# Optimization experiments

Measured on AMD Instinct MI355X. Metric: run time of the kernel, lower is better.

The kernel has to match this reference:

```python
import jax, jax.numpy as jnp
import numpy as np

TOP_K = 2
NUM_EXPERTS = 8


def setup_inputs() -> dict:
    key = jax.random.key(0)
    ks = jax.random.split(key, 8)
    B, S, H, F, E = 2, 2048, 1024, 4096, NUM_EXPERTS
    x = jax.random.normal(ks[0], (B, S, H), dtype=jnp.float32)
    # Router linear (TopKRouter): hidden -> num_experts
    Wr = jax.random.normal(ks[1], (H, E), dtype=jnp.float32) * 0.02
    br = jnp.zeros((E,), dtype=jnp.float32)
    # Per-expert FeedForwardExpert: Linear(H,F) -> relu -> Linear(F,H), stacked over experts
    W1 = jax.random.normal(ks[2], (E, H, F), dtype=jnp.float32) * 0.02
    b1 = jnp.zeros((E, F), dtype=jnp.float32)
    W2 = jax.random.normal(ks[3], (E, F, H), dtype=jnp.float32) * 0.02
    b2 = jnp.zeros((E, H), dtype=jnp.float32)
    return {"x": x, "Wr": Wr, "br": br, "W1": W1, "b1": b1, "W2": W2, "b2": b2}


def reference(x, Wr, br, W1, b1, W2, b2):
    """MoELayer.forward (eval mode, no dropout, capacity assumed sufficient so
    no random token dropping -- dropping in the original is randperm-based).
    Top-2 routing with renormalized top-k softmax probs, weighted combine."""
    B, S, H = x.shape
    E = Wr.shape[1]
    xf = x.reshape(-1, H)                                   # [T, H]
    logits = xf @ Wr + br                                   # [T, E]
    probs = jax.nn.softmax(logits, axis=-1)
    top_vals, top_idx = jax.lax.top_k(probs, TOP_K)         # [T, k]
    weights = top_vals / jnp.sum(top_vals, axis=-1, keepdims=True)
    # combine weight per (token, expert): sum over k slots assigned to e
    onehot = jax.nn.one_hot(top_idx, E, dtype=xf.dtype)     # [T, k, E]
    combine = jnp.einsum('tk,tke->te', weights, onehot)     # [T, E]
    out = jnp.zeros_like(xf)
    for e in range(E):  # small fixed loop over experts
        h = jax.nn.relu(xf @ W1[e] + b1[e]) @ W2[e] + b2[e]  # [T, H]
        out = out + combine[:, e:e + 1] * h
    return out.reshape(B, S, H)
```

## Files before the change

kernel.cpp:

```cpp
#include <hip/hip_runtime.h>

#define T_TOK 4096
#define H_DIM 1024
#define F_DIM 4096
#define E_NUM 8
#define R_TOT 8192
#define NT_MAX 72
#define R_CAP (NT_MAX * 128)

typedef short bf16x8 __attribute__((ext_vector_type(8)));
typedef float f32x4 __attribute__((ext_vector_type(4)));

__device__ inline unsigned int f2bf_u(float f) {
  unsigned int u = __builtin_bit_cast(unsigned int, f);
  return (u + 0x7FFFu + ((u >> 16) & 1u)) >> 16;
}
__device__ inline unsigned short f2bf(float f) { return (unsigned short)f2bf_u(f); }

__device__ inline void async16(const void* g, void* l) {
  __builtin_amdgcn_global_load_lds((const __attribute__((address_space(1))) void*)g,
                                   (__attribute__((address_space(3))) void*)l, 16, 0, 0);
}

__global__ __launch_bounds__(256) void prep_router_k(
    const float* __restrict__ W1, const float* __restrict__ W2,
    unsigned short* __restrict__ WT1, unsigned short* __restrict__ WT2,
    const float* __restrict__ x, const float* __restrict__ Wr,
    const float* __restrict__ br, int* __restrict__ ctrl,
    int* __restrict__ t2i, float* __restrict__ t2w) {
  int bid = blockIdx.x;
  if (bid < 1024) {
    int lane = threadIdx.x & 63;
    int wid  = threadIdx.x >> 6;
    int t = bid * 4 + wid;
    const float* xr = x + (size_t)t * H_DIM;
    double acc[E_NUM];
#pragma unroll
    for (int e = 0; e < E_NUM; e++) acc[e] = 0.0;
    for (int i = lane; i < H_DIM; i += 64) {
      float xv = xr[i];
      const float* wr = Wr + (size_t)i * E_NUM;
      float4 w0 = *(const float4*)wr;
      float4 w1 = *(const float4*)(wr + 4);
      acc[0] += (double)xv * w0.x; acc[1] += (double)xv * w0.y;
      acc[2] += (double)xv * w0.z; acc[3] += (double)xv * w0.w;
      acc[4] += (double)xv * w1.x; acc[5] += (double)xv * w1.y;
      acc[6] += (double)xv * w1.z; acc[7] += (double)xv * w1.w;
    }
#pragma unroll
    for (int e = 0; e < E_NUM; e++) {
      double v = acc[e];
      for (int off = 32; off > 0; off >>= 1) v += __shfl_down(v, off);
      acc[e] = v;
    }
    if (lane == 0) {
      float l[E_NUM];
#pragma unroll
      for (int e = 0; e < E_NUM; e++) l[e] = (float)acc[e] + br[e];
      int ia = 0; float la = l[0];
#pragma unroll
      for (int e = 1; e < E_NUM; e++) if (l[e] > la) { la = l[e]; ia = e; }
      int ib = -1; float lb = -3.4e38f;
#pragma unroll
      for (int e = 0; e < E_NUM; e++) if (e != ia && l[e] > lb) { lb = l[e]; ib = e; }
      float w0 = 1.f / (1.f + __expf(lb - la));
      float w1 = 1.f - w0;
      t2i[2 * t] = ia; t2i[2 * t + 1] = ib;
      t2w[2 * t] = w0; t2w[2 * t + 1] = w1;
      atomicAdd(&ctrl[ia], 1);
      atomicAdd(&ctrl[ib], 1);
    }
    return;
  }
  int b2 = bid - 1024;
  size_t mat = (size_t)H_DIM * F_DIM;
  const float* in; unsigned short* out; int R, C, c0, r0;
  if (b2 < 8192) {
    int e = b2 >> 10, t = b2 & 1023;
    in = W1 + e * mat; out = WT1 + e * mat; R = H_DIM; C = F_DIM;
    c0 = (t & 63) * 64; r0 = (t >> 6) * 64;
  } else {
    int b3 = b2 - 8192;
    int e = b3 >> 10, t = b3 & 1023;
    in = W2 + e * mat; out = WT2 + e * mat; R = F_DIM; C = H_DIM;
    c0 = (t & 15) * 64; r0 = (t >> 4) * 64;
  }
  __shared__ unsigned int tile32[32][66];
  {
    int rp = threadIdx.x >> 3;
    int tc = (threadIdx.x & 7) * 8;
    const float* s0 = in + (size_t)(r0 + 2 * rp) * C + c0 + tc;
    const float* s1 = s0 + C;
    float4 a0 = *(const float4*)s0, a1 = *(const float4*)(s0 + 4);
    float4 b0 = *(const float4*)s1, b1 = *(const float4*)(s1 + 4);
    uint4 u0, u1;
    u0.x = f2bf_u(a0.x) | (f2bf_u(b0.x) << 16);
    u0.y = f2bf_u(a0.y) | (f2bf_u(b0.y) << 16);
    u0.z = f2bf_u(a0.z) | (f2bf_u(b0.z) << 16);
    u0.w = f2bf_u(a0.w) | (f2bf_u(b0.w) << 16);
    u1.x = f2bf_u(a1.x) | (f2bf_u(b1.x) << 16);
    u1.y = f2bf_u(a1.y) | (f2bf_u(b1.y) << 16);
    u1.z = f2bf_u(a1.z) | (f2bf_u(b1.z) << 16);
    u1.w = f2bf_u(a1.w) | (f2bf_u(b1.w) << 16);
    *(uint4*)&tile32[rp][tc]     = u0;
    *(uint4*)&tile32[rp][tc + 4] = u1;
  }
  __syncthreads();
  {
    int col = threadIdx.x >> 2;
    int q   = (threadIdx.x & 3) * 2;
    unsigned short* ob = out + (size_t)(c0 + col) * R + r0;
#pragma unroll
    for (int w = 0; w < 2; w++) {
      int rw = (q + w) * 4;
      uint4 o;
      o.x = tile32[rw + 0][col];
      o.y = tile32[rw + 1][col];
      o.z = tile32[rw + 2][col];
      o.w = tile32[rw + 3][col];
      *(uint4*)(ob + (q + w) * 8) = o;
    }
  }
}

__global__ void scan_k(int* ctrl) {
  int lane = threadIdx.x;
  int c = (lane < 8) ? ctrl[lane] : 0;
  int tiles = (c + 127) >> 7;
  int x = tiles;
  for (int d = 1; d < 8; d <<= 1) {
    int y = __shfl_up(x, d);
    if (lane >= d) x += y;
  }
  int excl = x - tiles;
  if (lane < 8) {
    ctrl[8 + lane]  = excl * 128;
    ctrl[17 + lane] = excl * 128;
  }
  int tot = __shfl(x, 7);
  if (lane == 0) { ctrl[25] = tot; ctrl[16] = tot * 128; }
  int ex[8], tl[8];
#pragma unroll
  for (int e = 0; e < 8; e++) { ex[e] = __shfl(excl, e); tl[e] = __shfl(tiles, e); }
  for (int i = lane; i < tot; i += 64) {
    int myE = 0;
#pragma unroll
    for (int e = 0; e < 8; e++) if (i >= ex[e] && i < ex[e] + tl[e]) myE = e;
    ctrl[32 + 2 * i] = myE;
    ctrl[33 + 2 * i] = i * 128;
  }
}

__global__ __launch_bounds__(256) void assign_k(
    const int* __restrict__ t2i, int* __restrict__ ctrl, int* __restrict__ row_map) {
  int g = blockIdx.x * 256 + threadIdx.x;
  int lane = threadIdx.x & 63;
  int e = t2i[g];
  int row = 0;
#pragma unroll
  for (int ee = 0; ee < E_NUM; ee++) {
    unsigned long long mask = __ballot(e == ee);
    if (e == ee) {
      int leader = __ffsll((long long)mask) - 1;
      int cnt = __popcll(mask);
      int rank = __popcll(mask & ((lane == 63) ? ~0ull >> 1 << 1 >> 1 | ((1ull << 63) - 1) & ((1ull << lane) - 1) : ((1ull << lane) - 1)));
      int base = 0;
      if (lane == leader) base = atomicAdd(&ctrl[17 + ee], cnt);
      base = __shfl(base, leader);
      row = base + rank;
    }
  }
  row_map[g] = row;
}

__global__ __launch_bounds__(128) void gcopy_k(
    const float* __restrict__ x, const int* __restrict__ row_map,
    unsigned short* __restrict__ xg) {
  int bid = blockIdx.x;
  int row = row_map[bid];
  int t = bid >> 1;
  const float* src = x + (size_t)t * H_DIM + threadIdx.x * 8;
  unsigned short* dst = xg + (size_t)row * H_DIM + threadIdx.x * 8;
  float4 v0 = *(const float4*)src;
  float4 v1 = *(const float4*)(src + 4);
  uint4 o;
  o.x = f2bf_u(v0.x) | (f2bf_u(v0.y) << 16);
  o.y = f2bf_u(v0.z) | (f2bf_u(v0.w) << 16);
  o.z = f2bf_u(v1.x) | (f2bf_u(v1.y) << 16);
  o.w = f2bf_u(v1.z) | (f2bf_u(v1.w) << 16);
  *(uint4*)dst = o;
}

#define BAR() do { __builtin_amdgcn_sched_barrier(0); \
                   __builtin_amdgcn_s_barrier(); \
                   __builtin_amdgcn_sched_barrier(0); } while (0)

#define STG(gbase, kt, ebase, c) \
  async16((gbase) + (size_t)((c) * 32 + srcRow) * Kstr + (kt) + srcK8, \
          lds + (ebase) + (c) * 2048 + tid * 8)

#define LDU(ebase, row, koct) \
  (*(const bf16x8*)(lds + (ebase) + (((row) * 8 + ((koct) ^ ((row) & 7))) * 8)))

template <int MAP, bool RELU, bool OUTF32>
__global__ __launch_bounds__(256, 2) void gemm128_k(
    const int* __restrict__ ctrl, const unsigned short* __restrict__ A,
    const unsigned short* __restrict__ Bw, const float* __restrict__ bias,
    void* __restrict__ Cout, int Kstr, int N) {
  __shared__ unsigned short lds[32768];
  const int bid = blockIdx.x;
  int rt, bx;
  if (MAP == 1) {
    int wg = (bid & 7) * 288 + (bid >> 3);
    rt = wg >> 5; bx = wg & 31;
  } else {
    int wg = (bid & 7) * 72 + (bid >> 3);
    rt = wg >> 3; bx = wg & 7;
  }
  if (rt >= ctrl[25]) return;
  const int e    = ctrl[32 + 2 * rt];
  const int row0 = ctrl[33 + 2 * rt];
  const unsigned short* Ae = A + (size_t)row0 * Kstr;
  const unsigned short* Be = Bw + (size_t)e * ((size_t)N * Kstr) + (size_t)bx * 128 * Kstr;
  const int tid = threadIdx.x, lane = tid & 63;
  const int wid = tid >> 6, wm = wid >> 1, wn = wid & 1;
  const int lr = lane & 15, klane = lane >> 4;
  const int srcRow = tid >> 3;
  const int srcK8  = ((tid & 7) ^ (srcRow & 7)) * 8;
  const int NT = Kstr >> 6;

  f32x4 acc[4][4];
  f32x4 zero4 = {0.f, 0.f, 0.f, 0.f};
#pragma unroll
  for (int m = 0; m < 4; m++)
#pragma unroll
    for (int n = 0; n < 4; n++) acc[m][n] = zero4;

  {
    STG(Ae, 0, 0, 0); STG(Ae, 0, 0, 1); STG(Ae, 0, 0, 2); STG(Ae, 0, 0, 3);
    STG(Be, 0, 8192, 0); STG(Be, 0, 8192, 1); STG(Be, 0, 8192, 2); STG(Be, 0, 8192, 3);
    STG(Ae, 64, 16384, 0); STG(Ae, 64, 16384, 1); STG(Ae, 64, 16384, 2); STG(Ae, 64, 16384, 3);
    STG(Be, 64, 24576, 0); STG(Be, 64, 24576, 1); STG(Be, 64, 24576, 2); STG(Be, 64, 24576, 3);
    asm volatile("s_waitcnt vmcnt(8)" ::: "memory");
    BAR();
  }

  for (int t = 0; t < NT; t++) {
    const int cur = t & 1;
    const int abase = cur * 16384;
    const int bbase = abase + 8192;
    const int kt2 = min(t + 2, NT - 1) * 64;
    bf16x8 a[4][2], b[4][2];
#pragma unroll
    for (int m = 0; m < 4; m++) {
      int ar = wm * 64 + m * 16 + lr;
      a[m][0] = LDU(abase, ar, klane);
      a[m][1] = LDU(abase, ar, 4 + klane);
    }
#pragma unroll
    for (int n = 0; n < 4; n++) {
      int br = wn * 64 + n * 16 + lr;
      b[n][0] = LDU(bbase, br, klane);
      b[n][1] = LDU(bbase, br, 4 + klane);
    }
    asm volatile("s_waitcnt lgkmcnt(0)" ::: "memory");
    BAR();
    STG(Ae, kt2, abase, 0); STG(Ae, kt2, abase, 1);
    STG(Ae, kt2, abase, 2); STG(Ae, kt2, abase, 3);
    STG(Be, kt2, bbase, 0); STG(Be, kt2, bbase, 1);
    STG(Be, kt2, bbase, 2); STG(Be, kt2, bbase, 3);
    __builtin_amdgcn_s_setprio(1);
#pragma unroll
    for (int m = 0; m < 4; m++)
#pragma unroll
      for (int n = 0; n < 4; n++) {
        acc[m][n] = __builtin_amdgcn_mfma_f32_16x16x32_bf16(a[m][0], b[n][0], acc[m][n], 0, 0, 0);
        acc[m][n] = __builtin_amdgcn_mfma_f32_16x16x32_bf16(a[m][1], b[n][1], acc[m][n], 0, 0, 0);
      }
    __builtin_amdgcn_s_setprio(0);
    asm volatile("s_waitcnt vmcnt(8)" ::: "memory");
    BAR();
  }

  const int n0 = bx * 128;
  const float* be = bias + (size_t)e * N;
#pragma unroll
  for (int m = 0; m < 4; m++) {
#pragma unroll
    for (int q2 = 0; q2 < 4; q2++) {
      size_t ro = (size_t)(row0 + wm * 64 + m * 16 + (lane >> 4) * 4 + q2) * N;
#pragma unroll
      for (int n = 0; n < 4; n++) {
        int col = n0 + wn * 64 + n * 16 + lr;
        float v = acc[m][n][q2] + be[col];
        if (RELU) v = fmaxf(v, 0.f);
        if (OUTF32) ((float*)Cout)[ro + col] = v;
        else ((unsigned short*)Cout)[ro + col] = f2bf(v);
      }
    }
  }
}

__global__ __launch_bounds__(256) void combine_k(
    const float* __restrict__ y, const int* __restrict__ row_map,
    const float* __restrict__ t2w, float* __restrict__ out) {
  int t = blockIdx.x;
  int i = threadIdx.x * 4;
  int r0 = row_map[2 * t], r1 = row_map[2 * t + 1];
  float w0 = t2w[2 * t], w1 = t2w[2 * t + 1];
  float4 a = *(const float4*)(y + (size_t)r0 * H_DIM + i);
  float4 b = *(const float4*)(y + (size_t)r1 * H_DIM + i);
  float4 o;
  o.x = w0 * a.x + w1 * b.x;
  o.y = w0 * a.y + w1 * b.y;
  o.z = w0 * a.z + w1 * b.z;
  o.w = w0 * a.w + w1 * b.w;
  *(float4*)(out + (size_t)t * H_DIM + i) = o;
}

extern "C" void kernel_launch(void* const* d_in, const int* in_sizes, int n_in,
                              void* d_out, int out_size, void* d_ws, size_t ws_size,
                              hipStream_t stream) {
  const float* x  = (const float*)d_in[0];
  const float* Wr = (const float*)d_in[1];
  const float* br = (const float*)d_in[2];
  const float* W1 = (const float*)d_in[3];
  const float* b1 = (const float*)d_in[4];
  const float* W2 = (const float*)d_in[5];
  const float* b2 = (const float*)d_in[6];
  float* out = (float*)d_out;

  char* ws = (char*)d_ws;
  int*   ctrl    = (int*)ws;
  int*   t2i     = (int*)(ws + 4096);
  float* t2w     = (float*)(ws + 4096 + 32768);
  int*   row_map = (int*)(ws + 4096 + 65536);
  size_t off = (size_t)1 << 20;
  unsigned short* WT1 = (unsigned short*)(ws + off); off += (size_t)E_NUM * F_DIM * H_DIM * 2;
  unsigned short* WT2 = (unsigned short*)(ws + off); off += (size_t)E_NUM * H_DIM * F_DIM * 2;
  unsigned short* xg  = (unsigned short*)(ws + off); off += (size_t)R_CAP * H_DIM * 2;
  unsigned short* hb  = (unsigned short*)(ws + off); off += (size_t)R_CAP * F_DIM * 2;
  float*          yb  = (float*)(ws + off);          off += (size_t)R_CAP * H_DIM * 4;

  if (ws_size < off) {
    hipMemsetAsync(d_out, 0, (size_t)out_size * 4, stream);
    return;
  }

  hipMemsetAsync(ctrl, 0, 4096, stream);
  prep_router_k<<<dim3(17408), 256, 0, stream>>>(
      W1, W2, WT1, WT2, x, Wr, br, ctrl, t2i, t2w);
  scan_k<<<dim3(1), 64, 0, stream>>>(ctrl);
  assign_k<<<dim3(R_TOT / 256), 256, 0, stream>>>(t2i, ctrl, row_map);
  gcopy_k<<<dim3(R_TOT), 128, 0, stream>>>(x, row_map, xg);
  gemm128_k<1, true, false><<<dim3(2304), 256, 0, stream>>>(
      ctrl, xg, WT1, b1, hb, H_DIM, F_DIM);
  gemm128_k<2, false, true><<<dim3(576), 256, 0, stream>>>(
      ctrl, hb, WT2, b2, yb, F_DIM, H_DIM);
  combine_k<<<dim3(T_TOK), 256, 0, stream>>>(yb, row_map, t2w, out);
}
```

Measured before the change: 397.3 us.

## Pre-tile and pre-swizzle expert weights so GEMM B loads are contiguous

The weight-transpose prep kernel now writes each expert's bf16 weights in 128x64 tiles that are already XOR-swizzled to match the GEMM's LDS layout. The GEMM's B-operand stage then reads one contiguous 16 KB block per k-step instead of 128 rows strided by K. The router is also split into its own kernel, separate from the weight prep. The intent is more coalesced, DRAM-friendly B loads in both expert GEMMs, at the cost of one extra kernel launch and a fixed layout coupling between the prep and GEMM kernels.

```diff
diff --git a/kernel.cpp b/kernel.cpp
--- a/kernel.cpp
+++ b/kernel.cpp
@@ -22,69 +22,72 @@
                                    (__attribute__((address_space(3))) void*)l, 16, 0, 0);
 }
 
-__global__ __launch_bounds__(256) void prep_router_k(
-    const float* __restrict__ W1, const float* __restrict__ W2,
-    unsigned short* __restrict__ WT1, unsigned short* __restrict__ WT2,
+__global__ __launch_bounds__(256) void router_k(
     const float* __restrict__ x, const float* __restrict__ Wr,
     const float* __restrict__ br, int* __restrict__ ctrl,
     int* __restrict__ t2i, float* __restrict__ t2w) {
+  int lane = threadIdx.x & 63;
+  int wid  = threadIdx.x >> 6;
+  int t = blockIdx.x * 4 + wid;
+  const float* xr = x + (size_t)t * H_DIM;
+  double acc[E_NUM];
+#pragma unroll
+  for (int e = 0; e < E_NUM; e++) acc[e] = 0.0;
+  for (int i = lane; i < H_DIM; i += 64) {
+    float xv = xr[i];
+    const float* wr = Wr + (size_t)i * E_NUM;
+    float4 w0 = *(const float4*)wr;
+    float4 w1 = *(const float4*)(wr + 4);
+    acc[0] += (double)xv * w0.x; acc[1] += (double)xv * w0.y;
+    acc[2] += (double)xv * w0.z; acc[3] += (double)xv * w0.w;
+    acc[4] += (double)xv * w1.x; acc[5] += (double)xv * w1.y;
+    acc[6] += (double)xv * w1.z; acc[7] += (double)xv * w1.w;
+  }
+#pragma unroll
+  for (int e = 0; e < E_NUM; e++) {
+    double v = acc[e];
+    for (int off = 32; off > 0; off >>= 1) v += __shfl_down(v, off);
+    acc[e] = v;
+  }
+  if (lane == 0) {
+    float l[E_NUM];
+#pragma unroll
+    for (int e = 0; e < E_NUM; e++) l[e] = (float)acc[e] + br[e];
+    int ia = 0; float la = l[0];
+#pragma unroll
+    for (int e = 1; e < E_NUM; e++) if (l[e] > la) { la = l[e]; ia = e; }
+    int ib = -1; float lb = -3.4e38f;
+#pragma unroll
+    for (int e = 0; e < E_NUM; e++) if (e != ia && l[e] > lb) { lb = l[e]; ib = e; }
+    float w0 = 1.f / (1.f + __expf(lb - la));
+    float w1 = 1.f - w0;
+    t2i[2 * t] = ia; t2i[2 * t + 1] = ib;
+    t2w[2 * t] = w0; t2w[2 * t + 1] = w1;
+    atomicAdd(&ctrl[ia], 1);
+    atomicAdd(&ctrl[ib], 1);
+  }
+}
+
+__global__ __launch_bounds__(256) void prep_k(
+    const float* __restrict__ W1, const float* __restrict__ W2,
+    unsigned short* __restrict__ WT1, unsigned short* __restrict__ WT2) {
   int bid = blockIdx.x;
-  if (bid < 1024) {
-    int lane = threadIdx.x & 63;
-    int wid  = threadIdx.x >> 6;
-    int t = bid * 4 + wid;
-    const float* xr = x + (size_t)t * H_DIM;
-    double acc[E_NUM];
-#pragma unroll
-    for (int e = 0; e < E_NUM; e++) acc[e] = 0.0;
-    for (int i = lane; i < H_DIM; i += 64) {
-      float xv = xr[i];
-      const float* wr = Wr + (size_t)i * E_NUM;
-      float4 w0 = *(const float4*)wr;
-      float4 w1 = *(const float4*)(wr + 4);
-      acc[0] += (double)xv * w0.x; acc[1] += (double)xv * w0.y;
-      acc[2] += (double)xv * w0.z; acc[3] += (double)xv * w0.w;
-      acc[4] += (double)xv * w1.x; acc[5] += (double)xv * w1.y;
-      acc[6] += (double)xv * w1.z; acc[7] += (double)xv * w1.w;
-    }
-#pragma unroll
-    for (int e = 0; e < E_NUM; e++) {
-      double v = acc[e];
-      for (int off = 32; off > 0; off >>= 1) v += __shfl_down(v, off);
-      acc[e] = v;
-    }
-    if (lane == 0) {
-      float l[E_NUM];
-#pragma unroll
-      for (int e = 0; e < E_NUM; e++) l[e] = (float)acc[e] + br[e];
-      int ia = 0; float la = l[0];
-#pragma unroll
-      for (int e = 1; e < E_NUM; e++) if (l[e] > la) { la = l[e]; ia = e; }
-      int ib = -1; float lb = -3.4e38f;
-#pragma unroll
-      for (int e = 0; e < E_NUM; e++) if (e != ia && l[e] > lb) { lb = l[e]; ib = e; }
-      float w0 = 1.f / (1.f + __expf(lb - la));
-      float w1 = 1.f - w0;
-      t2i[2 * t] = ia; t2i[2 * t + 1] = ib;
-      t2w[2 * t] = w0; t2w[2 * t + 1] = w1;
-      atomicAdd(&ctrl[ia], 1);
-      atomicAdd(&ctrl[ib], 1);
-    }
-    return;
-  }
-  int b2 = bid - 1024;
   size_t mat = (size_t)H_DIM * F_DIM;
-  const float* in; unsigned short* out; int R, C, c0, r0;
-  if (b2 < 8192) {
-    int e = b2 >> 10, t = b2 & 1023;
-    in = W1 + e * mat; out = WT1 + e * mat; R = H_DIM; C = F_DIM;
-    c0 = (t & 63) * 64; r0 = (t >> 6) * 64;
+  const float* in; unsigned short* tb; int C, kt, bxp;
+  if (bid < 8192) {
+    int e = bid >> 10, t = bid & 1023;
+    in = W1 + e * mat; C = F_DIM;
+    kt = t >> 6; bxp = t & 63;
+    tb = WT1 + (((size_t)e * 16 + kt) * 32 + (bxp >> 1)) * 8192;
   } else {
-    int b3 = b2 - 8192;
+    int b3 = bid - 8192;
     int e = b3 >> 10, t = b3 & 1023;
-    in = W2 + e * mat; out = WT2 + e * mat; R = F_DIM; C = H_DIM;
-    c0 = (t & 15) * 64; r0 = (t >> 4) * 64;
-  }
+    in = W2 + e * mat; C = H_DIM;
+    kt = t >> 4; bxp = t & 15;
+    tb = WT2 + (((size_t)e * 64 + kt) * 8 + (bxp >> 1)) * 8192;
+  }
+  int r0 = kt * 64, c0 = bxp * 64;
+  int nl0 = (bxp & 1) * 64;
   __shared__ unsigned int tile32[32][66];
   {
     int rp = threadIdx.x >> 3;
@@ -109,16 +112,17 @@
   {
     int col = threadIdx.x >> 2;
     int q   = (threadIdx.x & 3) * 2;
-    unsigned short* ob = out + (size_t)(c0 + col) * R + r0;
+    unsigned short* ob = tb + (size_t)(nl0 + col) * 64;
 #pragma unroll
     for (int w = 0; w < 2; w++) {
-      int rw = (q + w) * 4;
-      uint4 o;
-      o.x = tile32[rw + 0][col];
-      o.y = tile32[rw + 1][col];
-      o.z = tile32[rw + 2][col];
-      o.w = tile32[rw + 3][col];
-      *(uint4*)(ob + (q + w) * 8) = o;
+      int o = q + w;
+      int slot = o ^ (col & 7);
+      uint4 v;
+      v.x = tile32[4 * o + 0][col];
+      v.y = tile32[4 * o + 1][col];
+      v.z = tile32[4 * o + 2][col];
+      v.w = tile32[4 * o + 3][col];
+      *(uint4*)(ob + slot * 8) = v;
     }
   }
 }
@@ -195,8 +199,12 @@
                    __builtin_amdgcn_s_barrier(); \
                    __builtin_amdgcn_sched_barrier(0); } while (0)
 
-#define STG(gbase, kt, ebase, c) \
-  async16((gbase) + (size_t)((c) * 32 + srcRow) * Kstr + (kt) + srcK8, \
+#define STGA(kt, ebase, c) \
+  async16(Ae + (size_t)((c) * 32 + srcRow) * Kstr + (kt) + srcK8, \
+          lds + (ebase) + (c) * 2048 + tid * 8)
+
+#define STGB(tb, ebase, c) \
+  async16(Be + (size_t)(tb) * tstride + (c) * 2048 + tid * 8, \
           lds + (ebase) + (c) * 2048 + tid * 8)
 
 #define LDU(ebase, row, koct) \
@@ -206,7 +214,7 @@
 __global__ __launch_bounds__(256, 2) void gemm128_k(
     const int* __restrict__ ctrl, const unsigned short* __restrict__ A,
     const unsigned short* __restrict__ Bw, const float* __restrict__ bias,
-    void* __restrict__ Cout, int Kstr, int N) {
+    void* __restrict__ Cout, int Kstr, int N, int tstride) {
   __shared__ unsigned short lds[32768];
   const int bid = blockIdx.x;
   int rt, bx;
@@ -221,7 +229,7 @@
   const int e    = ctrl[32 + 2 * rt];
   const int row0 = ctrl[33 + 2 * rt];
   const unsigned short* Ae = A + (size_t)row0 * Kstr;
-  const unsigned short* Be = Bw + (size_t)e * ((size_t)N * Kstr) + (size_t)bx * 128 * Kstr;
+  const unsigned short* Be = Bw + (size_t)e * ((size_t)N * Kstr) + (size_t)bx * 8192;
   const int tid = threadIdx.x, lane = tid & 63;
   const int wid = tid >> 6, wm = wid >> 1, wn = wid & 1;
   const int lr = lane & 15, klane = lane >> 4;
@@ -237,10 +245,10 @@
     for (int n = 0; n < 4; n++) acc[m][n] = zero4;
 
   {
-    STG(Ae, 0, 0, 0); STG(Ae, 0, 0, 1); STG(Ae, 0, 0, 2); STG(Ae, 0, 0, 3);
-    STG(Be, 0, 8192, 0); STG(Be, 0, 8192, 1); STG(Be, 0, 8192, 2); STG(Be, 0, 8192, 3);
-    STG(Ae, 64, 16384, 0); STG(Ae, 64, 16384, 1); STG(Ae, 64, 16384, 2); STG(Ae, 64, 16384, 3);
-    STG(Be, 64, 24576, 0); STG(Be, 64, 24576, 1); STG(Be, 64, 24576, 2); STG(Be, 64, 24576, 3);
+    STGA(0, 0, 0); STGA(0, 0, 1); STGA(0, 0, 2); STGA(0, 0, 3);
+    STGB(0, 8192, 0); STGB(0, 8192, 1); STGB(0, 8192, 2); STGB(0, 8192, 3);
+    STGA(64, 16384, 0); STGA(64, 16384, 1); STGA(64, 16384, 2); STGA(64, 16384, 3);
+    STGB(1, 24576, 0); STGB(1, 24576, 1); STGB(1, 24576, 2); STGB(1, 24576, 3);
     asm volatile("s_waitcnt vmcnt(8)" ::: "memory");
     BAR();
   }
@@ -249,7 +257,8 @@
     const int cur = t & 1;
     const int abase = cur * 16384;
     const int bbase = abase + 8192;
-    const int kt2 = min(t + 2, NT - 1) * 64;
+    const int tb2 = min(t + 2, NT - 1);
+    const int kt2 = tb2 * 64;
     bf16x8 a[4][2], b[4][2];
 #pragma unroll
     for (int m = 0; m < 4; m++) {
@@ -265,10 +274,10 @@
     }
     asm volatile("s_waitcnt lgkmcnt(0)" ::: "memory");
     BAR();
-    STG(Ae, kt2, abase, 0); STG(Ae, kt2, abase, 1);
-    STG(Ae, kt2, abase, 2); STG(Ae, kt2, abase, 3);
-    STG(Be, kt2, bbase, 0); STG(Be, kt2, bbase, 1);
-    STG(Be, kt2, bbase, 2); STG(Be, kt2, bbase, 3);
+    STGA(kt2, abase, 0); STGA(kt2, abase, 1);
+    STGA(kt2, abase, 2); STGA(kt2, abase, 3);
+    STGB(tb2, bbase, 0); STGB(tb2, bbase, 1);
+    STGB(tb2, bbase, 2); STGB(tb2, bbase, 3);
     __builtin_amdgcn_s_setprio(1);
 #pragma unroll
     for (int m = 0; m < 4; m++)
@@ -348,14 +357,14 @@
   }
 
   hipMemsetAsync(ctrl, 0, 4096, stream);
-  prep_router_k<<<dim3(17408), 256, 0, stream>>>(
-      W1, W2, WT1, WT2, x, Wr, br, ctrl, t2i, t2w);
+  router_k<<<dim3(T_TOK / 4), 256, 0, stream>>>(x, Wr, br, ctrl, t2i, t2w);
+  prep_k<<<dim3(16384), 256, 0, stream>>>(W1, W2, WT1, WT2);
   scan_k<<<dim3(1), 64, 0, stream>>>(ctrl);
   assign_k<<<dim3(R_TOT / 256), 256, 0, stream>>>(t2i, ctrl, row_map);
   gcopy_k<<<dim3(R_TOT), 128, 0, stream>>>(x, row_map, xg);
   gemm128_k<1, true, false><<<dim3(2304), 256, 0, stream>>>(
-      ctrl, xg, WT1, b1, hb, H_DIM, F_DIM);
+      ctrl, xg, WT1, b1, hb, H_DIM, F_DIM, 32 * 8192);
   gemm128_k<2, false, true><<<dim3(576), 256, 0, stream>>>(
-      ctrl, hb, WT2, b2, yb, F_DIM, H_DIM);
+      ctrl, hb, WT2, b2, yb, F_DIM, H_DIM, 8 * 8192);
   combine_k<<<dim3(T_TOK), 256, 0, stream>>>(yb, row_map, t2w, out);
 }
```

Measured after the change: 420.1 us. 1.06x slower.
